# Optimization experiments

Measured on AMD Instinct MI355X. Metric: run time of the kernel, lower is better.

## Reference

```python
import jax, jax.numpy as jnp
import numpy as np

N_NODES = 100000  # total nodes (60k type-a + 40k type-b)
N_EDGES = 3200000


def spmm(rows, cols, vals, x):
    # y[r] = sum_e vals[e] * x[cols[e]] for edges with rows[e] == r  (COO SpMM)
    return jax.ops.segment_sum(vals[:, None] * x[cols], rows, num_segments=N_NODES)


def setup_inputs() -> dict:
    key = jax.random.key(0)
    ks = jax.random.split(key, 12)
    d_a, d_b, n_hid, n_out = 256, 128, 256, 64
    s = lambda d: (1.0 / np.sqrt(d)).astype(np.float32)
    return {
        "x_a": jax.random.normal(ks[0], (60000, d_a), dtype=jnp.float32),
        "x_b": jax.random.normal(ks[1], (40000, d_b), dtype=jnp.float32),
        "rows": jax.random.randint(ks[2], (N_EDGES,), 0, N_NODES, dtype=jnp.int32),
        "cols": jax.random.randint(ks[3], (N_EDGES,), 0, N_NODES, dtype=jnp.int32),
        "vals": jax.random.uniform(ks[4], (N_EDGES,), dtype=jnp.float32),
        "W1a": jax.random.normal(ks[5], (d_a, n_hid), dtype=jnp.float32) * s(d_a),
        "b1a": jnp.zeros((n_hid,), dtype=jnp.float32),
        "W1b": jax.random.normal(ks[6], (d_b, n_hid), dtype=jnp.float32) * s(d_b),
        "b1b": jnp.zeros((n_hid,), dtype=jnp.float32),
        "Wf": jax.random.normal(ks[7], (n_hid, n_hid), dtype=jnp.float32) * s(n_hid),
        "bf": jnp.zeros((n_hid,), dtype=jnp.float32),
        "W2": jax.random.normal(ks[8], (n_hid, n_out), dtype=jnp.float32) * s(n_hid),
        "b2": jnp.zeros((n_out,), dtype=jnp.float32),
    }


def reference(x_a, x_b, rows, cols, vals, W1a, b1a, W1b, b1b, Wf, bf, W2, b2):
    # per-type Linear + ReLU (dropout p=0 -> identity in eval/reference)
    h_a = jax.nn.relu(x_a @ W1a + b1a)  # [60000, n_hid]
    h_b = jax.nn.relu(x_b @ W1b + b1b)  # [40000, n_hid]
    x = jnp.concatenate([h_a, h_b], axis=0)  # [N_NODES, n_hid]
    # hop - 1 = 1 intermediate hop: Linear -> SpMM -> ReLU
    x = x @ Wf + bf
    x = spmm(rows, cols, vals, x)
    x = jax.nn.relu(x)
    # output projection then final SpMM aggregation
    x = x @ W2 + b2
    x = spmm(rows, cols, vals, x)  # [N_NODES, n_out]
    return x
```

## Files before the change

### kernel.cpp

```cpp
#include <hip/hip_runtime.h>

#define NN 100000
#define NE 3200000
#define NA 60000
#define NB 40000
#define NHID 256
#define NOUT 64

#define RPB 64
#define NBUCK 1563
#define PBLK 256
#define CHUNK 12500

#define CVT_BLKS 20000
#define WT_BLKS 704
#define G1_BLKS 938
#define G2_BLKS 626
#define G3_BLKS 1564

typedef unsigned short u16;
typedef unsigned int u32;
typedef __attribute__((ext_vector_type(8))) short short8;
typedef __attribute__((ext_vector_type(4))) float f32x4;

__device__ __forceinline__ float bf2f(u16 u) {
  return __uint_as_float(((u32)u) << 16);
}
__device__ __forceinline__ u16 f2bf(float f) {
  u32 u = __float_as_uint(f);
  u32 r = (u + 0x7fffu + ((u >> 16) & 1u)) >> 16;
  return (u16)r;
}
__device__ __forceinline__ float i8f(u32 dw, int b) {
  return (float)((int)(dw << (24 - 8 * b)) >> 24);
}

__device__ __forceinline__ void gload_lds16(const void* gsrc, void* ldst) {
  __builtin_amdgcn_global_load_lds(
      (const __attribute__((address_space(1))) void*)gsrc,
      (__attribute__((address_space(3))) void*)ldst, 16, 0, 0);
}

template <int BN, int RELU_OUT, int QUANT>
__device__ __forceinline__ void gemm_body(
    int bx, int by, const u16* __restrict__ A, const u16* __restrict__ Bt,
    const float* __restrict__ bias, void* __restrict__ Cout,
    float* __restrict__ scales, int M, int N, int K, u16* As, u16* Bs) {
  constexpr int FI = (BN == 128) ? 4 : 2;
  constexpr int WROWS = FI * 16;

  const int tid = threadIdx.x;
  const int w = tid >> 6;
  const int lane = tid & 63;
  const int bm = bx * 128;
  const int bn = by * BN;
  const int wr = (BN == 128) ? (w >> 1) : w;
  const int wc = (BN == 128) ? (w & 1) : 0;

  f32x4 acc[FI][4];
#pragma unroll
  for (int i = 0; i < FI; ++i)
#pragma unroll
    for (int j = 0; j < 4; ++j) acc[i][j] = (f32x4)0.f;

  for (int k0 = 0; k0 < K; k0 += 32) {
#pragma unroll
    for (int s = 0; s < 2; ++s) {
      const int inst = w * 2 + s;
      const int row = inst * 16 + (lane >> 2);
      int rg = bm + row;
      if (rg > M - 1) rg = M - 1;
      const int c = (lane & 3) ^ ((row >> 1) & 3);
      gload_lds16(A + (size_t)rg * K + k0 + c * 8, &As[inst * 512]);
    }
    if (BN == 128) {
#pragma unroll
      for (int s = 0; s < 2; ++s) {
        const int inst = w * 2 + s;
        const int row = inst * 16 + (lane >> 2);
        const int c = (lane & 3) ^ ((row >> 1) & 3);
        gload_lds16(Bt + (size_t)(bn + row) * K + k0 + c * 8,
                    &Bs[inst * 512]);
      }
    } else {
      const int inst = w;
      const int row = inst * 16 + (lane >> 2);
      const int c = (lane & 3) ^ ((row >> 1) & 3);
      gload_lds16(Bt + (size_t)(bn + row) * K + k0 + c * 8, &Bs[inst * 512]);
    }
    __syncthreads();

    const int kc = lane >> 4;
    short8 af[FI], bfr[4];
#pragma unroll
    for (int i = 0; i < FI; ++i) {
      const int row = wr * WROWS + i * 16 + (lane & 15);
      const int ch = kc ^ ((row >> 1) & 3);
      af[i] = *reinterpret_cast<const short8*>(&As[row * 32 + ch * 8]);
    }
#pragma unroll
    for (int j = 0; j < 4; ++j) {
      const int row = wc * 64 + j * 16 + (lane & 15);
      const int ch = kc ^ ((row >> 1) & 3);
      bfr[j] = *reinterpret_cast<const short8*>(&Bs[row * 32 + ch * 8]);
    }
#pragma unroll
    for (int i = 0; i < FI; ++i)
#pragma unroll
      for (int j = 0; j < 4; ++j)
        acc[i][j] = __builtin_amdgcn_mfma_f32_16x16x32_bf16(af[i], bfr[j],
                                                            acc[i][j], 0, 0, 0);
    __syncthreads();
  }

  if constexpr (QUANT == 1) {
    float bv[4];
#pragma unroll
    for (int j = 0; j < 4; ++j)
      bv[j] = bias[bn + wc * 64 + j * 16 + (lane & 15)];
    const int g = (bn >> 6) + wc;
    u32* zq = (u32*)Cout;
#pragma unroll
    for (int i = 0; i < FI; ++i) {
#pragma unroll
      for (int r = 0; r < 4; ++r) {
        float o[4];
#pragma unroll
        for (int j = 0; j < 4; ++j) o[j] = acc[i][j][r] + bv[j];
        float am = fmaxf(fmaxf(fabsf(o[0]), fabsf(o[1])),
                         fmaxf(fabsf(o[2]), fabsf(o[3])));
#pragma unroll
        for (int mk = 1; mk < 16; mk <<= 1) am = fmaxf(am, __shfl_xor(am, mk));
        const float sinv = am > 0.f ? 127.f / am : 0.f;
        const float scv = am > 0.f ? am / 127.f : 0.f;
        const int q0 = __float2int_rn(o[0] * sinv);
        const int q1 = __float2int_rn(o[1] * sinv);
        const int q2 = __float2int_rn(o[2] * sinv);
        const int q3 = __float2int_rn(o[3] * sinv);
        const u32 dw = (q0 & 0xff) | ((q1 & 0xff) << 8) | ((q2 & 0xff) << 16) |
                       ((q3 & 0xff) << 24);
        const int row = bm + wr * WROWS + i * 16 + (lane >> 4) * 4 + r;
        if (row < M) {
          zq[(size_t)row * 64 + g * 16 + (lane & 15)] = dw;
          if ((lane & 15) == 0) scales[(size_t)row * 4 + g] = scv;
        }
      }
    }
  } else if constexpr (QUANT == 2) {
    float bv[4];
#pragma unroll
    for (int j = 0; j < 4; ++j) bv[j] = bias[j * 16 + (lane & 15)];
    u32* zq = (u32*)Cout;
#pragma unroll
    for (int i = 0; i < FI; ++i) {
#pragma unroll
      for (int r = 0; r < 4; ++r) {
        float o[4];
#pragma unroll
        for (int j = 0; j < 4; ++j) o[j] = acc[i][j][r] + bv[j];
        float am = fmaxf(fmaxf(fabsf(o[0]), fabsf(o[1])),
                         fmaxf(fabsf(o[2]), fabsf(o[3])));
#pragma unroll
        for (int mk = 1; mk < 16; mk <<= 1) am = fmaxf(am, __shfl_xor(am, mk));
        const float sinv = am > 0.f ? 127.f / am : 0.f;
        const float scv = am > 0.f ? am / 127.f : 0.f;
        const int q0 = __float2int_rn(o[0] * sinv);
        const int q1 = __float2int_rn(o[1] * sinv);
        const int q2 = __float2int_rn(o[2] * sinv);
        const int q3 = __float2int_rn(o[3] * sinv);
        const u32 dw = (q0 & 0xff) | ((q1 & 0xff) << 8) | ((q2 & 0xff) << 16) |
                       ((q3 & 0xff) << 24);
        const int row = bm + wr * WROWS + i * 16 + (lane >> 4) * 4 + r;
        if (row < M) {
          zq[(size_t)row * 16 + (lane & 15)] = dw;
          if ((lane & 15) == 0) scales[row] = scv;
        }
      }
    }
  } else {
    u16* C = (u16*)Cout;
#pragma unroll
    for (int i = 0; i < FI; ++i) {
#pragma unroll
      for (int j = 0; j < 4; ++j) {
        const int col = bn + wc * 64 + j * 16 + (lane & 15);
        const float bv = bias[col];
#pragma unroll
        for (int r = 0; r < 4; ++r) {
          const int row = bm + wr * WROWS + i * 16 + (lane >> 4) * 4 + r;
          if (row < M) {
            float o = acc[i][j][r] + bv;
            if (RELU_OUT) o = fmaxf(o, 0.f);
            C[(size_t)row * N + col] = f2bf(o);
          }
        }
      }
    }
  }
}

template <int BN, int RELU_OUT, int QUANT>
__global__ __launch_bounds__(256) void gemm_mfma(
    const u16* __restrict__ A, const u16* __restrict__ Bt,
    const float* __restrict__ bias, void* __restrict__ Cout,
    float* __restrict__ scales, int M, int N, int K) {
  __shared__ __align__(16) u16 As[128 * 32];
  __shared__ __align__(16) u16 Bs[BN * 32];
  gemm_body<BN, RELU_OUT, QUANT>(blockIdx.x, blockIdx.y, A, Bt, bias, Cout,
                                 scales, M, N, K, As, Bs);
}

__global__ __launch_bounds__(256) void prep(
    const float4* __restrict__ xa, ushort4* __restrict__ xab4,
    const float4* __restrict__ xb, ushort4* __restrict__ xbb4,
    const float* __restrict__ W1a, const float* __restrict__ W1b,
    const float* __restrict__ Wf, const float* __restrict__ W2,
    u16* __restrict__ W1at, u16* __restrict__ W1bt, u16* __restrict__ Wft,
    u16* __restrict__ W2t, const int* __restrict__ rows,
    int* __restrict__ cnt) {
  __shared__ int hsh[NBUCK];
  const int b = blockIdx.x;
  const int tid = threadIdx.x;
  if (b < CVT_BLKS) {
    const int i = b * 256 + tid;
    const int na4 = NA * 64;
    if (i < na4) {
      const float4 v = xa[i];
      ushort4 o;
      o.x = f2bf(v.x); o.y = f2bf(v.y); o.z = f2bf(v.z); o.w = f2bf(v.w);
      xab4[i] = o;
    } else {
      const int t = i - na4;
      const float4 v = xb[t];
      ushort4 o;
      o.x = f2bf(v.x); o.y = f2bf(v.y); o.z = f2bf(v.z); o.w = f2bf(v.w);
      xbb4[t] = o;
    }
  } else if (b < CVT_BLKS + WT_BLKS) {
    const int i = (b - CVT_BLKS) * 256 + tid;
    if (i < 65536) {
      const int n = i >> 8, k = i & 255;
      W1at[i] = f2bf(W1a[k * 256 + n]);
    } else if (i < 98304) {
      const int t = i - 65536;
      const int n = t >> 7, k = t & 127;
      W1bt[t] = f2bf(W1b[k * 256 + n]);
    } else if (i < 163840) {
      const int t = i - 98304;
      const int n = t >> 8, k = t & 255;
      Wft[t] = f2bf(Wf[k * 256 + n]);
    } else if (i < 180224) {
      const int t = i - 163840;
      const int n = t >> 8, p = t & 255;
      const int f = ((p >> 6) << 6) + ((p & 3) << 4) + ((p >> 2) & 15);
      W2t[t] = f2bf(W2[f * 64 + n]);
    }
  } else {
    const int blk = b - (CVT_BLKS + WT_BLKS);
    for (int i = tid; i < NBUCK; i += 256) hsh[i] = 0;
    __syncthreads();
    const int s = blk * CHUNK;
    const int e = s + CHUNK;
    for (int i = s + tid; i < e; i += 256) atomicAdd(&hsh[rows[i] >> 6], 1);
    __syncthreads();
    for (int i = tid; i < NBUCK; i += 256) cnt[i * PBLK + blk] = hsh[i];
  }
}

__global__ __launch_bounds__(256) void gemm12_s1(
    const u16* __restrict__ xab, const u16* __restrict__ W1at,
    const float* __restrict__ b1a, const u16* __restrict__ xbb,
    const u16* __restrict__ W1bt, const float* __restrict__ b1b,
    u16* __restrict__ h, int* __restrict__ cnt, int* __restrict__ btot) {
  __shared__ __align__(16) u16 As[128 * 32];
  __shared__ __align__(16) u16 Bs[128 * 32];
  const int b = blockIdx.x;
  if (b < G1_BLKS) {
    gemm_body<128, 1, 0>(b % 469, b / 469, xab, W1at, b1a, h, nullptr, NA,
                         NHID, 256, As, Bs);
  } else if (b < G1_BLKS + G2_BLKS) {
    const int t = b - G1_BLKS;
    gemm_body<128, 1, 0>(t % 313, t / 313, xbb, W1bt, b1b,
                         h + (size_t)NA * NHID, nullptr, NB, NHID, 128, As,
                         Bs);
  } else {
    int* lds = (int*)As;
    const int bu = b - (G1_BLKS + G2_BLKS);
    const int t = threadIdx.x;
    const int v = cnt[bu * PBLK + t];
    lds[t] = v;
    __syncthreads();
#pragma unroll
    for (int off = 1; off < 256; off <<= 1) {
      const int x = (t >= off) ? lds[t - off] : 0;
      __syncthreads();
      lds[t] += x;
      __syncthreads();
    }
    cnt[bu * PBLK + t] = lds[t] - v;
    if (t == 255) btot[bu] = lds[255];
  }
}

__global__ __launch_bounds__(256) void gemm3_s2(
    const u16* __restrict__ h, const u16* __restrict__ Wft,
    const float* __restrict__ bfv, u32* __restrict__ zq,
    float* __restrict__ zscale, const int* __restrict__ btot,
    int* __restrict__ bstart) {
  __shared__ __align__(16) u16 As[128 * 32];
  __shared__ __align__(16) u16 Bs[128 * 32];
  const int b = blockIdx.x;
  if (b < G3_BLKS) {
    gemm_body<128, 0, 1>(b % 782, b / 782, h, Wft, bfv, zq, zscale, NN, NHID,
                         256, As, Bs);
  } else {
    int* lds = (int*)As;
    const int t = threadIdx.x;
    int carry = 0;
    for (int base = 0; base < NBUCK; base += 256) {
      const int i = base + t;
      const int v = (i < NBUCK) ? btot[i] : 0;
      lds[t] = v;
      __syncthreads();
#pragma unroll
      for (int off = 1; off < 256; off <<= 1) {
        const int x = (t >= off) ? lds[t - off] : 0;
        __syncthreads();
        lds[t] += x;
        __syncthreads();
      }
      const int excl = lds[t] - v;
      const int tot = lds[255];
      if (i < NBUCK) bstart[i] = carry + excl;
      __syncthreads();
      carry += tot;
    }
    if (t == 0) bstart[NBUCK] = NE;
  }
}

__global__ __launch_bounds__(256) void p3_scatter(
    const int* __restrict__ rows, const int* __restrict__ cols,
    const float* __restrict__ vals, const int* __restrict__ cnt,
    const int* __restrict__ bstart, int2* __restrict__ edges) {
  __shared__ int lcur[NBUCK];
  const int tid = threadIdx.x;
  const int blk = blockIdx.x;
  for (int bu = tid; bu < NBUCK; bu += 256)
    lcur[bu] = bstart[bu] + cnt[bu * PBLK + blk];
  __syncthreads();
  const int s = blk * CHUNK;
  const int e = s + CHUNK;
  for (int i = s + tid; i < e; i += 256) {
    const int r = rows[i];
    const int bu = r >> 6;
    const int lr = r & 63;
    const int pos = atomicAdd(&lcur[bu], 1);
    edges[pos] = make_int2(cols[i] | (lr << 17), __float_as_int(vals[i]));
  }
}

__global__ __launch_bounds__(256) void sort_bucket(
    const int* __restrict__ bstart, const int2* __restrict__ edges,
    int2* __restrict__ edges2, int* __restrict__ rptr) {
  __shared__ int hist[RPB];
  __shared__ int sc[RPB];
  __shared__ int cur[RPB];
  const int bu = blockIdx.x;
  const int t = threadIdx.x;
  const int s = bstart[bu], e = bstart[bu + 1];
  if (t < RPB) hist[t] = 0;
  __syncthreads();
  for (int i = s + t; i < e; i += 256)
    atomicAdd(&hist[(edges[i].x >> 17) & 63], 1);
  __syncthreads();
  const int hv = (t < RPB) ? hist[t] : 0;
  if (t < RPB) sc[t] = hv;
  __syncthreads();
#pragma unroll
  for (int off = 1; off < RPB; off <<= 1) {
    const int x = (t >= off && t < RPB) ? sc[t - off] : 0;
    __syncthreads();
    if (t < RPB) sc[t] += x;
    __syncthreads();
  }
  if (t < RPB) {
    const int base = s + sc[t] - hv;
    cur[t] = base;
    const int grow = bu * RPB + t;
    if (grow < NN) rptr[grow] = base;
  }
  if (bu == 0 && t == 0) rptr[NN] = NE;
  __syncthreads();
  for (int i = s + t; i < e; i += 256) {
    const int2 ed = edges[i];
    const int lr = (ed.x >> 17) & 63;
    const int pos = atomicAdd(&cur[lr], 1);
    edges2[pos] = make_int2(ed.x & 0x1FFFF, ed.y);
  }
}

__global__ __launch_bounds__(256) void spmm256_q8(
    const int* __restrict__ ptr, const int2* __restrict__ edges,
    const u32* __restrict__ Zq, const float* __restrict__ scales,
    u16* __restrict__ Yb) {
  const int wid = (int)((blockIdx.x * (size_t)256 + threadIdx.x) >> 6);
  const int lane = threadIdx.x & 63;
  if (wid >= NN) return;
  const int s = ptr[wid], e = ptr[wid + 1];
  const int gsel = lane >> 4;
  float a0 = 0.f, a1 = 0.f, a2 = 0.f, a3 = 0.f;
  int j = s;
  for (; j + 7 < e; j += 8) {
    int2 ed[8];
#pragma unroll
    for (int q = 0; q < 8; ++q) ed[q] = edges[j + q];
    u32 dw[8];
    float sc[8];
#pragma unroll
    for (int q = 0; q < 8; ++q) {
      dw[q] = Zq[(size_t)ed[q].x * 64 + lane];
      sc[q] = scales[(size_t)ed[q].x * 4 + gsel];
    }
#pragma unroll
    for (int q = 0; q < 8; ++q) {
      const float vs = __int_as_float(ed[q].y) * sc[q];
      a0 += vs * i8f(dw[q], 0);
      a1 += vs * i8f(dw[q], 1);
      a2 += vs * i8f(dw[q], 2);
      a3 += vs * i8f(dw[q], 3);
    }
  }
  for (; j < e; ++j) {
    const int2 e0 = edges[j];
    const u32 dw = Zq[(size_t)e0.x * 64 + lane];
    const float vs =
        __int_as_float(e0.y) * scales[(size_t)e0.x * 4 + gsel];
    a0 += vs * i8f(dw, 0);
    a1 += vs * i8f(dw, 1);
    a2 += vs * i8f(dw, 2);
    a3 += vs * i8f(dw, 3);
  }
  ushort4 o;
  o.x = f2bf(fmaxf(a0, 0.f));
  o.y = f2bf(fmaxf(a1, 0.f));
  o.z = f2bf(fmaxf(a2, 0.f));
  o.w = f2bf(fmaxf(a3, 0.f));
  reinterpret_cast<ushort4*>(Yb + (size_t)wid * 256)[lane] = o;
}

__global__ __launch_bounds__(256) void spmm64_q8(
    const int* __restrict__ ptr, const int2* __restrict__ edges,
    const u32* __restrict__ Z2q, const float* __restrict__ zsc2,
    float* __restrict__ Y) {
  const int wid = (int)((blockIdx.x * (size_t)256 + threadIdx.x) >> 6);
  const int lane = threadIdx.x & 63;
  if (wid >= NN) return;
  const int s = ptr[wid], e = ptr[wid + 1];
  const int dwi = lane & 15;
  const int byi = lane >> 4;
  float acc = 0.f;
  int j = s;
  for (; j + 7 < e; j += 8) {
    int2 ed[8];
#pragma unroll
    for (int q = 0; q < 8; ++q) ed[q] = edges[j + q];
    u32 dw[8];
    float sc[8];
#pragma unroll
    for (int q = 0; q < 8; ++q) {
      dw[q] = Z2q[(size_t)ed[q].x * 16 + dwi];
      sc[q] = zsc2[ed[q].x];
    }
#pragma unroll
    for (int q = 0; q < 8; ++q)
      acc += __int_as_float(ed[q].y) * sc[q] * i8f(dw[q], byi);
  }
  for (; j < e; ++j) {
    const int2 e0 = edges[j];
    const u32 dw = Z2q[(size_t)e0.x * 16 + dwi];
    acc += __int_as_float(e0.y) * zsc2[e0.x] * i8f(dw, byi);
  }
  Y[(size_t)wid * 64 + lane] = acc;
}

extern "C" void kernel_launch(void* const* d_in, const int* in_sizes, int n_in,
                              void* d_out, int out_size, void* d_ws,
                              size_t ws_size, hipStream_t stream) {
  const float* x_a  = (const float*)d_in[0];
  const float* x_b  = (const float*)d_in[1];
  const int*   rows = (const int*)d_in[2];
  const int*   cols = (const int*)d_in[3];
  const float* vals = (const float*)d_in[4];
  const float* W1a  = (const float*)d_in[5];
  const float* b1a  = (const float*)d_in[6];
  const float* W1b  = (const float*)d_in[7];
  const float* b1b  = (const float*)d_in[8];
  const float* Wf   = (const float*)d_in[9];
  const float* bf   = (const float*)d_in[10];
  const float* W2   = (const float*)d_in[11];
  const float* b2   = (const float*)d_in[12];
  float* out = (float*)d_out;

  char* p = (char*)d_ws;
  u16* h    = (u16*)p;  p += (size_t)NN * NHID * 2;
  u32* zq   = (u32*)p;  p += (size_t)NN * 64 * 4;
  float* zscale = (float*)p; p += (size_t)NN * 4 * 4;
  u32* z2q  = (u32*)p;  p += (size_t)NN * 16 * 4;
  float* zsc2 = (float*)p; p += (size_t)NN * 4;
  u16* xab  = (u16*)p;  p += (size_t)NA * 256 * 2;
  u16* xbb  = (u16*)p;  p += (size_t)NB * 128 * 2;
  u16* W1at = (u16*)p;  p += 256 * 256 * 2;
  u16* W1bt = (u16*)p;  p += 256 * 128 * 2;
  u16* Wft  = (u16*)p;  p += 256 * 256 * 2;
  u16* W2t  = (u16*)p;  p += 64 * 256 * 2;
  int2* edges = (int2*)p; p += (size_t)NE * 8;
  int* cnt    = (int*)p;  p += (size_t)NBUCK * PBLK * 4;
  int* btot   = (int*)p;  p += (size_t)((NBUCK + 3) & ~3) * 4;
  int* bstart = (int*)p;  p += (size_t)((NBUCK + 4) & ~3) * 4;
  int* rptr   = (int*)p;  p += (size_t)(NN + 4) * 4;
  u16* s1b = h;
  int2* edges2 = (int2*)xab;

  prep<<<CVT_BLKS + WT_BLKS + PBLK, 256, 0, stream>>>(
      (const float4*)x_a, (ushort4*)xab, (const float4*)x_b, (ushort4*)xbb,
      W1a, W1b, Wf, W2, W1at, W1bt, Wft, W2t, rows, cnt);

  gemm12_s1<<<G1_BLKS + G2_BLKS + NBUCK, 256, 0, stream>>>(
      xab, W1at, b1a, xbb, W1bt, b1b, h, cnt, btot);

  gemm3_s2<<<G3_BLKS + 1, 256, 0, stream>>>(h, Wft, bf, zq, zscale, btot,
                                            bstart);

  p3_scatter<<<PBLK, 256, 0, stream>>>(rows, cols, vals, cnt, bstart, edges);
  sort_bucket<<<NBUCK, 256, 0, stream>>>(bstart, edges, edges2, rptr);

  spmm256_q8<<<(NN * 64 + 255) / 256, 256, 0, stream>>>(rptr, edges2, zq,
                                                        zscale, s1b);
  gemm_mfma<64, 0, 2><<<dim3((NN + 127) / 128, 1), 256, 0, stream>>>(
      s1b, W2t, b2, z2q, zsc2, NN, NOUT, 256);
  spmm64_q8<<<(NN * 64 + 255) / 256, 256, 0, stream>>>(rptr, edges2, z2q,
                                                       zsc2, out);
}
```

Measured before the change: 491.9 us.

## Fuse fp32-to-bf16 input conversion into first GEMM and merge scatter into gemm3

The separate conversion pass that wrote bf16 copies of x_a and x_b is removed. The first-layer GEMM now loads fp32 rows directly, converts them in registers and stores them swizzled into LDS. The edge scatter kernel is folded into the gemm3 launch: each scatter block recomputes the bucket-start prefix scan locally, so it no longer needs a separate launch or a dependency on the global bstart. This saves a full read/write pass over the input features and one kernel launch. In exchange, A-tile loads in the GEMM become synchronous register loads instead of async LDS loads, and 256 blocks each redo the bucket scan.

```diff
diff --git a/kernel.cpp b/kernel.cpp
--- a/kernel.cpp
+++ b/kernel.cpp
@@ -12,7 +12,6 @@
 #define PBLK 256
 #define CHUNK 12500
 
-#define CVT_BLKS 20000
 #define WT_BLKS 704
 #define G1_BLKS 938
 #define G2_BLKS 626
@@ -199,6 +198,99 @@
   }
 }
 
+__device__ __forceinline__ void gemm_af32(
+    int bx, int by, const float* __restrict__ Af, const u16* __restrict__ Bt,
+    const float* __restrict__ bias, u16* __restrict__ C, int M, int K,
+    u16* As, u16* Bs) {
+  constexpr int N = 256;
+  const int tid = threadIdx.x;
+  const int w = tid >> 6;
+  const int lane = tid & 63;
+  const int bm = bx * 128;
+  const int bn = by * 128;
+  const int wr = w >> 1;
+  const int wc = w & 1;
+
+  f32x4 acc[4][4];
+#pragma unroll
+  for (int i = 0; i < 4; ++i)
+#pragma unroll
+    for (int j = 0; j < 4; ++j) acc[i][j] = (f32x4)0.f;
+
+  const int arow = tid >> 1;
+  const int ahalf = tid & 1;
+  int arg = bm + arow;
+  if (arg > M - 1) arg = M - 1;
+  const int asw = (arow >> 1) & 3;
+
+  for (int k0 = 0; k0 < K; k0 += 32) {
+#pragma unroll
+    for (int s = 0; s < 2; ++s) {
+      const int inst = w * 2 + s;
+      const int row = inst * 16 + (lane >> 2);
+      const int c = (lane & 3) ^ ((row >> 1) & 3);
+      gload_lds16(Bt + (size_t)(bn + row) * K + k0 + c * 8, &Bs[inst * 512]);
+    }
+    {
+      const float4* src = reinterpret_cast<const float4*>(
+          Af + (size_t)arg * K + k0 + ahalf * 16);
+      const float4 v0 = src[0], v1 = src[1], v2 = src[2], v3 = src[3];
+      short8 lo, hi;
+      lo[0] = (short)f2bf(v0.x); lo[1] = (short)f2bf(v0.y);
+      lo[2] = (short)f2bf(v0.z); lo[3] = (short)f2bf(v0.w);
+      lo[4] = (short)f2bf(v1.x); lo[5] = (short)f2bf(v1.y);
+      lo[6] = (short)f2bf(v1.z); lo[7] = (short)f2bf(v1.w);
+      hi[0] = (short)f2bf(v2.x); hi[1] = (short)f2bf(v2.y);
+      hi[2] = (short)f2bf(v2.z); hi[3] = (short)f2bf(v2.w);
+      hi[4] = (short)f2bf(v3.x); hi[5] = (short)f2bf(v3.y);
+      hi[6] = (short)f2bf(v3.z); hi[7] = (short)f2bf(v3.w);
+      short8* dst = reinterpret_cast<short8*>(As + arow * 32);
+      dst[(ahalf * 2) ^ asw] = lo;
+      dst[(ahalf * 2 + 1) ^ asw] = hi;
+    }
+    __syncthreads();
+
+    const int kc = lane >> 4;
+    short8 af[4], bfr[4];
+#pragma unroll
+    for (int i = 0; i < 4; ++i) {
+      const int row = wr * 64 + i * 16 + (lane & 15);
+      const int ch = kc ^ ((row >> 1) & 3);
+      af[i] = *reinterpret_cast<const short8*>(&As[row * 32 + ch * 8]);
+    }
+#pragma unroll
+    for (int j = 0; j < 4; ++j) {
+      const int row = wc * 64 + j * 16 + (lane & 15);
+      const int ch = kc ^ ((row >> 1) & 3);
+      bfr[j] = *reinterpret_cast<const short8*>(&Bs[row * 32 + ch * 8]);
+    }
+#pragma unroll
+    for (int i = 0; i < 4; ++i)
+#pragma unroll
+      for (int j = 0; j < 4; ++j)
+        acc[i][j] = __builtin_amdgcn_mfma_f32_16x16x32_bf16(af[i], bfr[j],
+                                                            acc[i][j], 0, 0, 0);
+    __syncthreads();
+  }
+
+#pragma unroll
+  for (int i = 0; i < 4; ++i) {
+#pragma unroll
+    for (int j = 0; j < 4; ++j) {
+      const int col = bn + wc * 64 + j * 16 + (lane & 15);
+      const float bv = bias[col];
+#pragma unroll
+      for (int r = 0; r < 4; ++r) {
+        const int row = bm + wr * 64 + i * 16 + (lane >> 4) * 4 + r;
+        if (row < M) {
+          float o = fmaxf(acc[i][j][r] + bv, 0.f);
+          C[(size_t)row * N + col] = f2bf(o);
+        }
+      }
+    }
+  }
+}
+
 template <int BN, int RELU_OUT, int QUANT>
 __global__ __launch_bounds__(256) void gemm_mfma(
     const u16* __restrict__ A, const u16* __restrict__ Bt,
@@ -211,8 +303,6 @@
 }
 
 __global__ __launch_bounds__(256) void prep(
-    const float4* __restrict__ xa, ushort4* __restrict__ xab4,
-    const float4* __restrict__ xb, ushort4* __restrict__ xbb4,
     const float* __restrict__ W1a, const float* __restrict__ W1b,
     const float* __restrict__ Wf, const float* __restrict__ W2,
     u16* __restrict__ W1at, u16* __restrict__ W1bt, u16* __restrict__ Wft,
@@ -221,23 +311,8 @@
   __shared__ int hsh[NBUCK];
   const int b = blockIdx.x;
   const int tid = threadIdx.x;
-  if (b < CVT_BLKS) {
+  if (b < WT_BLKS) {
     const int i = b * 256 + tid;
-    const int na4 = NA * 64;
-    if (i < na4) {
-      const float4 v = xa[i];
-      ushort4 o;
-      o.x = f2bf(v.x); o.y = f2bf(v.y); o.z = f2bf(v.z); o.w = f2bf(v.w);
-      xab4[i] = o;
-    } else {
-      const int t = i - na4;
-      const float4 v = xb[t];
-      ushort4 o;
-      o.x = f2bf(v.x); o.y = f2bf(v.y); o.z = f2bf(v.z); o.w = f2bf(v.w);
-      xbb4[t] = o;
-    }
-  } else if (b < CVT_BLKS + WT_BLKS) {
-    const int i = (b - CVT_BLKS) * 256 + tid;
     if (i < 65536) {
       const int n = i >> 8, k = i & 255;
       W1at[i] = f2bf(W1a[k * 256 + n]);
@@ -256,7 +331,7 @@
       W2t[t] = f2bf(W2[f * 64 + n]);
     }
   } else {
-    const int blk = b - (CVT_BLKS + WT_BLKS);
+    const int blk = b - WT_BLKS;
     for (int i = tid; i < NBUCK; i += 256) hsh[i] = 0;
     __syncthreads();
     const int s = blk * CHUNK;
@@ -268,21 +343,19 @@
 }
 
 __global__ __launch_bounds__(256) void gemm12_s1(
-    const u16* __restrict__ xab, const u16* __restrict__ W1at,
-    const float* __restrict__ b1a, const u16* __restrict__ xbb,
+    const float* __restrict__ xa, const u16* __restrict__ W1at,
+    const float* __restrict__ b1a, const float* __restrict__ xb,
     const u16* __restrict__ W1bt, const float* __restrict__ b1b,
     u16* __restrict__ h, int* __restrict__ cnt, int* __restrict__ btot) {
   __shared__ __align__(16) u16 As[128 * 32];
   __shared__ __align__(16) u16 Bs[128 * 32];
   const int b = blockIdx.x;
   if (b < G1_BLKS) {
-    gemm_body<128, 1, 0>(b % 469, b / 469, xab, W1at, b1a, h, nullptr, NA,
-                         NHID, 256, As, Bs);
+    gemm_af32(b % 469, b / 469, xa, W1at, b1a, h, NA, 256, As, Bs);
   } else if (b < G1_BLKS + G2_BLKS) {
     const int t = b - G1_BLKS;
-    gemm_body<128, 1, 0>(t % 313, t / 313, xbb, W1bt, b1b,
-                         h + (size_t)NA * NHID, nullptr, NB, NHID, 128, As,
-                         Bs);
+    gemm_af32(t % 313, t / 313, xb, W1bt, b1b, h + (size_t)NA * NHID, NB, 128,
+              As, Bs);
   } else {
     int* lds = (int*)As;
     const int bu = b - (G1_BLKS + G2_BLKS);
@@ -302,20 +375,22 @@
   }
 }
 
-__global__ __launch_bounds__(256) void gemm3_s2(
+__global__ __launch_bounds__(256) void gemm3_s2_p3(
     const u16* __restrict__ h, const u16* __restrict__ Wft,
     const float* __restrict__ bfv, u32* __restrict__ zq,
     float* __restrict__ zscale, const int* __restrict__ btot,
-    int* __restrict__ bstart) {
+    int* __restrict__ bstart, const int* __restrict__ rows,
+    const int* __restrict__ cols, const float* __restrict__ vals,
+    const int* __restrict__ cnt, int2* __restrict__ edges) {
   __shared__ __align__(16) u16 As[128 * 32];
   __shared__ __align__(16) u16 Bs[128 * 32];
   const int b = blockIdx.x;
+  const int t = threadIdx.x;
   if (b < G3_BLKS) {
     gemm_body<128, 0, 1>(b % 782, b / 782, h, Wft, bfv, zq, zscale, NN, NHID,
                          256, As, Bs);
-  } else {
+  } else if (b == G3_BLKS) {
     int* lds = (int*)As;
-    const int t = threadIdx.x;
     int carry = 0;
     for (int base = 0; base < NBUCK; base += 256) {
       const int i = base + t;
@@ -336,27 +411,37 @@
       carry += tot;
     }
     if (t == 0) bstart[NBUCK] = NE;
-  }
-}
-
-__global__ __launch_bounds__(256) void p3_scatter(
-    const int* __restrict__ rows, const int* __restrict__ cols,
-    const float* __restrict__ vals, const int* __restrict__ cnt,
-    const int* __restrict__ bstart, int2* __restrict__ edges) {
-  __shared__ int lcur[NBUCK];
-  const int tid = threadIdx.x;
-  const int blk = blockIdx.x;
-  for (int bu = tid; bu < NBUCK; bu += 256)
-    lcur[bu] = bstart[bu] + cnt[bu * PBLK + blk];
-  __syncthreads();
-  const int s = blk * CHUNK;
-  const int e = s + CHUNK;
-  for (int i = s + tid; i < e; i += 256) {
-    const int r = rows[i];
-    const int bu = r >> 6;
-    const int lr = r & 63;
-    const int pos = atomicAdd(&lcur[bu], 1);
-    edges[pos] = make_int2(cols[i] | (lr << 17), __float_as_int(vals[i]));
+  } else {
+    const int blk = b - (G3_BLKS + 1);
+    int* lbs = (int*)As;
+    int* tmp = (int*)Bs;
+    int carry = 0;
+    for (int base = 0; base < NBUCK; base += 256) {
+      const int i = base + t;
+      const int v = (i < NBUCK) ? btot[i] : 0;
+      tmp[t] = v;
+      __syncthreads();
+#pragma unroll
+      for (int off = 1; off < 256; off <<= 1) {
+        const int x = (t >= off) ? tmp[t - off] : 0;
+        __syncthreads();
+        tmp[t] += x;
+        __syncthreads();
+      }
+      if (i < NBUCK) lbs[i] = carry + tmp[t] - v;
+      const int tot = tmp[255];
+      __syncthreads();
+      carry += tot;
+    }
+    for (int bu = t; bu < NBUCK; bu += 256) lbs[bu] += cnt[bu * PBLK + blk];
+    __syncthreads();
+    const int s = blk * CHUNK;
+    const int e = s + CHUNK;
+    for (int i = s + t; i < e; i += 256) {
+      const int r = rows[i];
+      const int pos = atomicAdd(&lbs[r >> 6], 1);
+      edges[pos] = make_int2(cols[i] | ((r & 63) << 17), __float_as_int(vals[i]));
+    }
   }
 }
 
@@ -508,8 +593,7 @@
   float* zscale = (float*)p; p += (size_t)NN * 4 * 4;
   u32* z2q  = (u32*)p;  p += (size_t)NN * 16 * 4;
   float* zsc2 = (float*)p; p += (size_t)NN * 4;
-  u16* xab  = (u16*)p;  p += (size_t)NA * 256 * 2;
-  u16* xbb  = (u16*)p;  p += (size_t)NB * 128 * 2;
+  int2* edges2 = (int2*)p; p += (size_t)NE * 8;
   u16* W1at = (u16*)p;  p += 256 * 256 * 2;
   u16* W1bt = (u16*)p;  p += 256 * 128 * 2;
   u16* Wft  = (u16*)p;  p += 256 * 256 * 2;
@@ -520,19 +604,16 @@
   int* bstart = (int*)p;  p += (size_t)((NBUCK + 4) & ~3) * 4;
   int* rptr   = (int*)p;  p += (size_t)(NN + 4) * 4;
   u16* s1b = h;
-  int2* edges2 = (int2*)xab;
-
-  prep<<<CVT_BLKS + WT_BLKS + PBLK, 256, 0, stream>>>(
-      (const float4*)x_a, (ushort4*)xab, (const float4*)x_b, (ushort4*)xbb,
-      W1a, W1b, Wf, W2, W1at, W1bt, Wft, W2t, rows, cnt);
+
+  prep<<<WT_BLKS + PBLK, 256, 0, stream>>>(W1a, W1b, Wf, W2, W1at, W1bt, Wft,
+                                           W2t, rows, cnt);
 
   gemm12_s1<<<G1_BLKS + G2_BLKS + NBUCK, 256, 0, stream>>>(
-      xab, W1at, b1a, xbb, W1bt, b1b, h, cnt, btot);
-
-  gemm3_s2<<<G3_BLKS + 1, 256, 0, stream>>>(h, Wft, bf, zq, zscale, btot,
-                                            bstart);
-
-  p3_scatter<<<PBLK, 256, 0, stream>>>(rows, cols, vals, cnt, bstart, edges);
+      x_a, W1at, b1a, x_b, W1bt, b1b, h, cnt, btot);
+
+  gemm3_s2_p3<<<G3_BLKS + 1 + PBLK, 256, 0, stream>>>(
+      h, Wft, bf, zq, zscale, btot, bstart, rows, cols, vals, cnt, edges);
+
   sort_bucket<<<NBUCK, 256, 0, stream>>>(bstart, edges, edges2, rptr);
 
   spmm256_q8<<<(NN * 64 + 255) / 256, 256, 0, stream>>>(rptr, edges2, zq,
```

Result: faster. 479.4 us (-2.5%).
